# Kernel optimization log

Measured on AMD Instinct MI355X. Metric: run time of the kernel, lower is better.

## Reference

```python
import jax, jax.numpy as jnp
import numpy as np

EPS = 1e-5

def activation_quant(x):
    # per-token absmax int8 quant-dequant (BitNet b1.58)
    scale = 127.0 / jnp.clip(jnp.max(jnp.abs(x), axis=-1, keepdims=True), EPS)
    q = jnp.clip(jnp.round(x * scale), -128.0, 127.0) / scale
    return q

def weight_quant(w):
    # per-tensor ternary quant-dequant: scale by 1/mean|w|, round, clamp to {-1,0,1}
    scale = 1.0 / jnp.clip(jnp.mean(jnp.abs(w)), EPS)
    q = jnp.clip(jnp.round(w * scale), -1.0, 1.0) / scale
    return q

def bitlinear(x, w):
    # x: [b, s, in], w: [out, in] (nn.Linear layout)
    return jnp.einsum('bsi,oi->bso', activation_quant(x), weight_quant(w))

def setup_inputs() -> dict:
    key = jax.random.key(0)
    k1, k2, k3, k4 = jax.random.split(key, 4)
    B, S, H, I = 2, 2048, 4096, 11008
    x = jax.random.normal(k1, (B, S, H), dtype=jnp.float32)
    w_gate = jax.random.normal(k2, (I, H), dtype=jnp.float32) * (1.0 / np.sqrt(H))
    w_up = jax.random.normal(k3, (I, H), dtype=jnp.float32) * (1.0 / np.sqrt(H))
    w_down = jax.random.normal(k4, (H, I), dtype=jnp.float32) * (1.0 / np.sqrt(I))
    return {"x": x, "w_gate": w_gate, "w_up": w_up, "w_down": w_down}

def reference(x, w_gate, w_up, w_down):
    g = bitlinear(x, w_gate)           # [B, S, I]
    u = bitlinear(x, w_up)             # [B, S, I]
    h = jnp.square(jax.nn.relu(g)) * u  # ReLU^2 gating
    return bitlinear(h, w_down)        # [B, S, H]
```

## Files before the change

### kernel.cpp

```cpp
#include <hip/hip_runtime.h>
#include <stdint.h>

#define TOKENS 4096
#define HDIM   4096
#define IDIM   11008
#define WELEMS 45088768L

using i32x4 = __attribute__((ext_vector_type(4))) int;
using s8x16 = __attribute__((ext_vector_type(16))) signed char;

__device__ __forceinline__ void async_load16(const void* g, void* l) {
  __builtin_amdgcn_global_load_lds(
      (const __attribute__((address_space(1))) void*)g,
      (__attribute__((address_space(3))) void*)l, 16, 0, 0);
}

__global__ __launch_bounds__(256) void wsum_kernel(
    const float* __restrict__ w0, const float* __restrict__ w1,
    const float* __restrict__ w2, double* __restrict__ dsum) {
  const float* w = (blockIdx.y == 0) ? w0 : (blockIdx.y == 1) ? w1 : w2;
  const long n4 = WELEMS / 4;
  long i = (long)blockIdx.x * blockDim.x + threadIdx.x;
  const long stride = (long)gridDim.x * blockDim.x;
  double s = 0.0;
  for (; i < n4; i += stride) {
    float4 v = ((const float4*)w)[i];
    s += (double)fabsf(v.x); s += (double)fabsf(v.y);
    s += (double)fabsf(v.z); s += (double)fabsf(v.w);
  }
  __shared__ double red[256];
  red[threadIdx.x] = s;
  __syncthreads();
  for (int off = 128; off; off >>= 1) {
    if (threadIdx.x < (unsigned)off) red[threadIdx.x] += red[threadIdx.x + off];
    __syncthreads();
  }
  if (threadIdx.x == 0) atomicAdd(&dsum[blockIdx.y], red[0]);
}

__global__ void wscale_kernel(const double* __restrict__ dsum, double* __restrict__ wsc) {
  int i = threadIdx.x;
  if (i < 3) {
    double mean = dsum[i] / (double)WELEMS;
    wsc[i] = 1.0 / fmax(mean, 1e-5);
  }
}

__global__ __launch_bounds__(256) void wquant_kernel(
    const float* __restrict__ w0, const float* __restrict__ w1, const float* __restrict__ w2,
    int8_t* __restrict__ q0, int8_t* __restrict__ q1, int8_t* __restrict__ q2,
    const double* __restrict__ wsc) {
  const int wi = blockIdx.y;
  const float* w = (wi == 0) ? w0 : (wi == 1) ? w1 : w2;
  int8_t* q = (wi == 0) ? q0 : (wi == 1) ? q1 : q2;
  const double sc = wsc[wi];
  long c = (long)blockIdx.x * blockDim.x + threadIdx.x;
  if (c * 16 >= WELEMS) return;
  const float4* src = (const float4*)(w + c * 16);
  s8x16 outv;
  #pragma unroll
  for (int j = 0; j < 4; ++j) {
    float4 v = src[j];
    double t0 = rint((double)v.x * sc); t0 = fmin(fmax(t0, -1.0), 1.0);
    double t1 = rint((double)v.y * sc); t1 = fmin(fmax(t1, -1.0), 1.0);
    double t2 = rint((double)v.z * sc); t2 = fmin(fmax(t2, -1.0), 1.0);
    double t3 = rint((double)v.w * sc); t3 = fmin(fmax(t3, -1.0), 1.0);
    outv[j*4+0] = (signed char)(int)t0; outv[j*4+1] = (signed char)(int)t1;
    outv[j*4+2] = (signed char)(int)t2; outv[j*4+3] = (signed char)(int)t3;
  }
  *(s8x16*)(q + c * 16) = outv;
}

__global__ __launch_bounds__(256) void xquant_kernel(
    const float* __restrict__ x, int8_t* __restrict__ xq, double* __restrict__ sx) {
  const int row = blockIdx.x;
  const float* xr = x + (long)row * HDIM;
  const float4* xr4 = (const float4*)xr;
  float m = 0.f;
  for (int i = threadIdx.x; i < HDIM / 4; i += 256) {
    float4 v = xr4[i];
    m = fmaxf(m, fmaxf(fmaxf(fabsf(v.x), fabsf(v.y)), fmaxf(fabsf(v.z), fabsf(v.w))));
  }
  __shared__ float red[256];
  red[threadIdx.x] = m;
  __syncthreads();
  for (int off = 128; off; off >>= 1) {
    if (threadIdx.x < (unsigned)off) red[threadIdx.x] = fmaxf(red[threadIdx.x], red[threadIdx.x + off]);
    __syncthreads();
  }
  __shared__ double s_sc;
  if (threadIdx.x == 0) {
    double sc = 127.0 / fmax((double)red[0], 1e-5);
    sx[row] = sc;
    s_sc = sc;
  }
  __syncthreads();
  const double sc = s_sc;
  s8x16 outv;
  #pragma unroll
  for (int j = 0; j < 4; ++j) {
    float4 v = xr4[threadIdx.x * 4 + j];
    double t0 = rint((double)v.x * sc); t0 = fmin(fmax(t0, -128.0), 127.0);
    double t1 = rint((double)v.y * sc); t1 = fmin(fmax(t1, -128.0), 127.0);
    double t2 = rint((double)v.z * sc); t2 = fmin(fmax(t2, -128.0), 127.0);
    double t3 = rint((double)v.w * sc); t3 = fmin(fmax(t3, -128.0), 127.0);
    outv[j*4+0] = (signed char)(int)t0; outv[j*4+1] = (signed char)(int)t1;
    outv[j*4+2] = (signed char)(int)t2; outv[j*4+3] = (signed char)(int)t3;
  }
  *(s8x16*)(xq + (long)row * HDIM + threadIdx.x * 16) = outv;
}

__global__ __launch_bounds__(256, 2) void gemm1_kernel(
    const int8_t* __restrict__ Aq, const int8_t* __restrict__ Bg, const int8_t* __restrict__ Bu,
    const double* __restrict__ sx, const double* __restrict__ wsc,
    float* __restrict__ H, unsigned int* __restrict__ hmax) {
  __shared__ __align__(16) int8_t As[128 * 64];
  __shared__ __align__(16) int8_t Bsg[128 * 64];
  __shared__ __align__(16) int8_t Bsu[128 * 64];
  __shared__ unsigned int smax[128];

  const int tid = threadIdx.x;
  const int l = tid & 63;
  const int wv = tid >> 6;
  const int wm = (wv >> 1) * 64;
  const int wn = (wv & 1) * 64;
  const int row0 = blockIdx.y * 128;
  const int col0 = blockIdx.x * 128;

  i32x4 accg[4][4], accu[4][4];
  #pragma unroll
  for (int i = 0; i < 4; i++)
    #pragma unroll
    for (int j = 0; j < 4; j++) { accg[i][j] = i32x4{0,0,0,0}; accu[i][j] = i32x4{0,0,0,0}; }

  const int off0 = tid * 16;
  const int rs = off0 >> 6;
  const int cs = off0 & 63;

  for (int k0 = 0; k0 < HDIM; k0 += 64) {
    #pragma unroll
    for (int s = 0; s < 2; ++s) {
      const int off = off0 + s * 4096;
      const int r = rs + s * 64;
      const long ga = (long)(row0 + r) * HDIM + k0 + cs;
      const long gb = (long)(col0 + r) * HDIM + k0 + cs;
      async_load16(Aq + ga, As + off);
      async_load16(Bg + gb, Bsg + off);
      async_load16(Bu + gb, Bsu + off);
    }
    __syncthreads();
    const int kq = (l >> 4) * 16;
    const int mr = l & 15;
    i32x4 af[4], bgf[4], buf_[4];
    #pragma unroll
    for (int t = 0; t < 4; t++) af[t] = *(const i32x4*)(As + (wm + t * 16 + mr) * 64 + kq);
    #pragma unroll
    for (int t = 0; t < 4; t++) {
      bgf[t] = *(const i32x4*)(Bsg + (wn + t * 16 + mr) * 64 + kq);
      buf_[t] = *(const i32x4*)(Bsu + (wn + t * 16 + mr) * 64 + kq);
    }
    #pragma unroll
    for (int mt = 0; mt < 4; mt++)
      #pragma unroll
      for (int nt = 0; nt < 4; nt++) {
        accg[mt][nt] = __builtin_amdgcn_mfma_i32_16x16x64_i8(af[mt], bgf[nt], accg[mt][nt], 0, 0, 0);
        accu[mt][nt] = __builtin_amdgcn_mfma_i32_16x16x64_i8(af[mt], buf_[nt], accu[mt][nt], 0, 0, 0);
      }
    __syncthreads();
  }

  if (tid < 128) smax[tid] = 0u;
  __syncthreads();
  const double swg = wsc[0], swu = wsc[1];
  #pragma unroll
  for (int mt = 0; mt < 4; mt++) {
    #pragma unroll
    for (int r = 0; r < 4; r++) {
      const int grow = wm + mt * 16 + (l >> 4) * 4 + r;
      const long growg = row0 + grow;
      const double sxr = sx[growg];
      const double dg = 1.0 / (sxr * swg);
      const double du = 1.0 / (sxr * swu);
      float am = 0.f;
      #pragma unroll
      for (int nt = 0; nt < 4; nt++) {
        const float g = (float)((double)accg[mt][nt][r] * dg);
        const float u = (float)((double)accu[mt][nt][r] * du);
        const float gr = g > 0.f ? g * g : 0.f;
        const float h = gr * u;
        H[growg * IDIM + col0 + wn + nt * 16 + (l & 15)] = h;
        am = fmaxf(am, fabsf(h));
      }
      atomicMax(&smax[grow], __float_as_uint(am));
    }
  }
  __syncthreads();
  if (tid < 128) atomicMax(&hmax[row0 + tid], smax[tid]);
}

__global__ __launch_bounds__(256) void hquant_kernel(
    const float* __restrict__ H, int8_t* __restrict__ hq, const unsigned int* __restrict__ hmax) {
  const long c = (long)blockIdx.x * blockDim.x + threadIdx.x;
  const long nchunks = (long)TOKENS * IDIM / 16;
  if (c >= nchunks) return;
  const int row = (int)(c / (IDIM / 16));
  const double sc = 127.0 / fmax((double)__uint_as_float(hmax[row]), 1e-5);
  const float4* src = (const float4*)(H + c * 16);
  s8x16 outv;
  #pragma unroll
  for (int j = 0; j < 4; ++j) {
    float4 v = src[j];
    double t0 = rint((double)v.x * sc); t0 = fmin(fmax(t0, -128.0), 127.0);
    double t1 = rint((double)v.y * sc); t1 = fmin(fmax(t1, -128.0), 127.0);
    double t2 = rint((double)v.z * sc); t2 = fmin(fmax(t2, -128.0), 127.0);
    double t3 = rint((double)v.w * sc); t3 = fmin(fmax(t3, -128.0), 127.0);
    outv[j*4+0] = (signed char)(int)t0; outv[j*4+1] = (signed char)(int)t1;
    outv[j*4+2] = (signed char)(int)t2; outv[j*4+3] = (signed char)(int)t3;
  }
  *(s8x16*)(hq + c * 16) = outv;
}

__global__ __launch_bounds__(256, 2) void gemm2_kernel(
    const int8_t* __restrict__ Aq, const int8_t* __restrict__ Bq,
    const unsigned int* __restrict__ hmax, const double* __restrict__ wsc,
    float* __restrict__ out) {
  __shared__ __align__(16) int8_t As[128 * 64];
  __shared__ __align__(16) int8_t Bs[128 * 64];

  const int tid = threadIdx.x;
  const int l = tid & 63;
  const int wv = tid >> 6;
  const int wm = (wv >> 1) * 64;
  const int wn = (wv & 1) * 64;
  const int row0 = blockIdx.y * 128;
  const int col0 = blockIdx.x * 128;

  i32x4 acc[4][4];
  #pragma unroll
  for (int i = 0; i < 4; i++)
    #pragma unroll
    for (int j = 0; j < 4; j++) acc[i][j] = i32x4{0,0,0,0};

  const int off0 = tid * 16;
  const int rs = off0 >> 6;
  const int cs = off0 & 63;

  for (int k0 = 0; k0 < IDIM; k0 += 64) {
    #pragma unroll
    for (int s = 0; s < 2; ++s) {
      const int off = off0 + s * 4096;
      const int r = rs + s * 64;
      const long ga = (long)(row0 + r) * IDIM + k0 + cs;
      const long gb = (long)(col0 + r) * IDIM + k0 + cs;
      async_load16(Aq + ga, As + off);
      async_load16(Bq + gb, Bs + off);
    }
    __syncthreads();
    const int kq = (l >> 4) * 16;
    const int mr = l & 15;
    i32x4 af[4], bf[4];
    #pragma unroll
    for (int t = 0; t < 4; t++) af[t] = *(const i32x4*)(As + (wm + t * 16 + mr) * 64 + kq);
    #pragma unroll
    for (int t = 0; t < 4; t++) bf[t] = *(const i32x4*)(Bs + (wn + t * 16 + mr) * 64 + kq);
    #pragma unroll
    for (int mt = 0; mt < 4; mt++)
      #pragma unroll
      for (int nt = 0; nt < 4; nt++)
        acc[mt][nt] = __builtin_amdgcn_mfma_i32_16x16x64_i8(af[mt], bf[nt], acc[mt][nt], 0, 0, 0);
    __syncthreads();
  }

  const double swd = wsc[2];
  #pragma unroll
  for (int mt = 0; mt < 4; mt++) {
    #pragma unroll
    for (int r = 0; r < 4; r++) {
      const int grow = wm + mt * 16 + (l >> 4) * 4 + r;
      const long growg = row0 + grow;
      const double shr = 127.0 / fmax((double)__uint_as_float(hmax[growg]), 1e-5);
      const double inv = 1.0 / (shr * swd);
      #pragma unroll
      for (int nt = 0; nt < 4; nt++)
        out[growg * HDIM + col0 + wn + nt * 16 + (l & 15)] = (float)((double)acc[mt][nt][r] * inv);
    }
  }
}

extern "C" void kernel_launch(void* const* d_in, const int* in_sizes, int n_in,
                              void* d_out, int out_size, void* d_ws, size_t ws_size,
                              hipStream_t stream) {
  const float* x  = (const float*)d_in[0];
  const float* wg = (const float*)d_in[1];
  const float* wu = (const float*)d_in[2];
  const float* wd = (const float*)d_in[3];
  float* out = (float*)d_out;

  char* ws = (char*)d_ws;
  double*   dsum  = (double*)ws;
  double*   wsc   = (double*)(ws + 32);
  double*   sx    = (double*)(ws + 64);
  unsigned* hmaxb = (unsigned*)(ws + 64 + TOKENS * 8);
  int8_t*   xq    = (int8_t*)(ws + 131072);
  int8_t*   wqg   = xq + (long)TOKENS * HDIM;
  int8_t*   wqu   = wqg + WELEMS;
  int8_t*   wqd   = wqu + WELEMS;
  int8_t*   hq    = wqd + WELEMS;
  float*    H     = (float*)(hq + WELEMS);
  const size_t needed = 131072 + (size_t)TOKENS * HDIM + 4 * (size_t)WELEMS
                      + (size_t)TOKENS * IDIM * sizeof(float);
  if (ws_size < needed) {
    hipMemsetAsync(d_out, 0, (size_t)out_size * sizeof(float), stream);
    return;
  }

  hipMemsetAsync(ws, 0, 65536, stream);

  { dim3 g(1024, 3); wsum_kernel<<<g, 256, 0, stream>>>(wg, wu, wd, dsum); }
  wscale_kernel<<<1, 64, 0, stream>>>(dsum, wsc);
  { dim3 g((unsigned)(WELEMS / (256 * 16)), 3);
    wquant_kernel<<<g, 256, 0, stream>>>(wg, wu, wd, wqg, wqu, wqd, wsc); }
  xquant_kernel<<<TOKENS, 256, 0, stream>>>(x, xq, sx);
  { dim3 g(IDIM / 128, TOKENS / 128);
    gemm1_kernel<<<g, 256, 0, stream>>>(xq, wqg, wqu, sx, wsc, H, hmaxb); }
  hquant_kernel<<<(unsigned)((long)TOKENS * IDIM / 16 / 256), 256, 0, stream>>>(H, hq, hmaxb);
  { dim3 g(HDIM / 128, TOKENS / 128);
    gemm2_kernel<<<g, 256, 0, stream>>>(hq, wqd, hmaxb, wsc, out); }
}
```

Measured before the change: 1.386 ms.

## Use 32x32x32 int8 MFMA with XOR-swizzled LDS and swapped grid order

```diff
diff --git a/kernel.cpp b/kernel.cpp
--- a/kernel.cpp
+++ b/kernel.cpp
@@ -6,8 +6,9 @@
 #define IDIM   11008
 #define WELEMS 45088768L
 
-using i32x4 = __attribute__((ext_vector_type(4))) int;
-using s8x16 = __attribute__((ext_vector_type(16))) signed char;
+using i32x4  = __attribute__((ext_vector_type(4))) int;
+using i32x16 = __attribute__((ext_vector_type(16))) int;
+using s8x16  = __attribute__((ext_vector_type(16))) signed char;
 
 __device__ __forceinline__ void async_load16(const void* g, void* l) {
   __builtin_amdgcn_global_load_lds(
@@ -120,52 +121,65 @@
   __shared__ unsigned int smax[128];
 
   const int tid = threadIdx.x;
-  const int l = tid & 63;
+  const int l  = tid & 63;
   const int wv = tid >> 6;
   const int wm = (wv >> 1) * 64;
   const int wn = (wv & 1) * 64;
-  const int row0 = blockIdx.y * 128;
-  const int col0 = blockIdx.x * 128;
-
-  i32x4 accg[4][4], accu[4][4];
-  #pragma unroll
-  for (int i = 0; i < 4; i++)
-    #pragma unroll
-    for (int j = 0; j < 4; j++) { accg[i][j] = i32x4{0,0,0,0}; accu[i][j] = i32x4{0,0,0,0}; }
+  const int lr = l & 31;
+  const int lh = l >> 5;
+  const int row0 = blockIdx.x * 128;
+  const int col0 = blockIdx.y * 128;
+
+  i32x16 accg[2][2], accu[2][2];
+  #pragma unroll
+  for (int i = 0; i < 2; i++)
+    #pragma unroll
+    for (int j = 0; j < 2; j++) {
+      #pragma unroll
+      for (int e = 0; e < 16; e++) { accg[i][j][e] = 0; accu[i][j][e] = 0; }
+    }
 
   const int off0 = tid * 16;
-  const int rs = off0 >> 6;
-  const int cs = off0 & 63;
+  const int rs = tid >> 2;
+  const int ch = tid & 3;
+  const int csw = (ch ^ ((rs >> 1) & 3)) * 16;
 
   for (int k0 = 0; k0 < HDIM; k0 += 64) {
     #pragma unroll
     for (int s = 0; s < 2; ++s) {
       const int off = off0 + s * 4096;
       const int r = rs + s * 64;
-      const long ga = (long)(row0 + r) * HDIM + k0 + cs;
-      const long gb = (long)(col0 + r) * HDIM + k0 + cs;
+      const long ga = (long)(row0 + r) * HDIM + k0 + csw;
+      const long gb = (long)(col0 + r) * HDIM + k0 + csw;
       async_load16(Aq + ga, As + off);
       async_load16(Bg + gb, Bsg + off);
       async_load16(Bu + gb, Bsu + off);
     }
     __syncthreads();
-    const int kq = (l >> 4) * 16;
-    const int mr = l & 15;
-    i32x4 af[4], bgf[4], buf_[4];
-    #pragma unroll
-    for (int t = 0; t < 4; t++) af[t] = *(const i32x4*)(As + (wm + t * 16 + mr) * 64 + kq);
-    #pragma unroll
-    for (int t = 0; t < 4; t++) {
-      bgf[t] = *(const i32x4*)(Bsg + (wn + t * 16 + mr) * 64 + kq);
-      buf_[t] = *(const i32x4*)(Bsu + (wn + t * 16 + mr) * 64 + kq);
-    }
-    #pragma unroll
-    for (int mt = 0; mt < 4; mt++)
-      #pragma unroll
-      for (int nt = 0; nt < 4; nt++) {
-        accg[mt][nt] = __builtin_amdgcn_mfma_i32_16x16x64_i8(af[mt], bgf[nt], accg[mt][nt], 0, 0, 0);
-        accu[mt][nt] = __builtin_amdgcn_mfma_i32_16x16x64_i8(af[mt], buf_[nt], accu[mt][nt], 0, 0, 0);
-      }
+    #pragma unroll
+    for (int ks = 0; ks < 2; ++ks) {
+      const int c0 = ks * 2 + lh;
+      i32x4 af[2], bgf[2], buf_[2];
+      #pragma unroll
+      for (int t = 0; t < 2; t++) {
+        const int ra = wm + t * 32 + lr;
+        af[t] = *(const i32x4*)(As + ra * 64 + ((c0 ^ ((ra >> 1) & 3)) * 16));
+      }
+      #pragma unroll
+      for (int t = 0; t < 2; t++) {
+        const int rb = wn + t * 32 + lr;
+        const int cb = (c0 ^ ((rb >> 1) & 3)) * 16;
+        bgf[t]  = *(const i32x4*)(Bsg + rb * 64 + cb);
+        buf_[t] = *(const i32x4*)(Bsu + rb * 64 + cb);
+      }
+      #pragma unroll
+      for (int mt = 0; mt < 2; mt++)
+        #pragma unroll
+        for (int nt = 0; nt < 2; nt++) {
+          accg[mt][nt] = __builtin_amdgcn_mfma_i32_32x32x32_i8(af[mt], bgf[nt],  accg[mt][nt], 0, 0, 0);
+          accu[mt][nt] = __builtin_amdgcn_mfma_i32_32x32x32_i8(af[mt], buf_[nt], accu[mt][nt], 0, 0, 0);
+        }
+    }
     __syncthreads();
   }
 
@@ -173,25 +187,25 @@
   __syncthreads();
   const double swg = wsc[0], swu = wsc[1];
   #pragma unroll
-  for (int mt = 0; mt < 4; mt++) {
-    #pragma unroll
-    for (int r = 0; r < 4; r++) {
-      const int grow = wm + mt * 16 + (l >> 4) * 4 + r;
-      const long growg = row0 + grow;
+  for (int mt = 0; mt < 2; mt++) {
+    #pragma unroll
+    for (int reg = 0; reg < 16; reg++) {
+      const int rl = wm + mt * 32 + (reg & 3) + 8 * (reg >> 2) + 4 * lh;
+      const long growg = row0 + rl;
       const double sxr = sx[growg];
       const double dg = 1.0 / (sxr * swg);
       const double du = 1.0 / (sxr * swu);
       float am = 0.f;
       #pragma unroll
-      for (int nt = 0; nt < 4; nt++) {
-        const float g = (float)((double)accg[mt][nt][r] * dg);
-        const float u = (float)((double)accu[mt][nt][r] * du);
+      for (int nt = 0; nt < 2; nt++) {
+        const float g = (float)((double)accg[mt][nt][reg] * dg);
+        const float u = (float)((double)accu[mt][nt][reg] * du);
         const float gr = g > 0.f ? g * g : 0.f;
         const float h = gr * u;
-        H[growg * IDIM + col0 + wn + nt * 16 + (l & 15)] = h;
+        H[growg * IDIM + col0 + wn + nt * 32 + lr] = h;
         am = fmaxf(am, fabsf(h));
       }
-      atomicMax(&smax[grow], __float_as_uint(am));
+      atomicMax(&smax[rl], __float_as_uint(am));
     }
   }
   __syncthreads();
@@ -228,61 +242,75 @@
   __shared__ __align__(16) int8_t Bs[128 * 64];
 
   const int tid = threadIdx.x;
-  const int l = tid & 63;
+  const int l  = tid & 63;
   const int wv = tid >> 6;
   const int wm = (wv >> 1) * 64;
   const int wn = (wv & 1) * 64;
-  const int row0 = blockIdx.y * 128;
-  const int col0 = blockIdx.x * 128;
-
-  i32x4 acc[4][4];
-  #pragma unroll
-  for (int i = 0; i < 4; i++)
-    #pragma unroll
-    for (int j = 0; j < 4; j++) acc[i][j] = i32x4{0,0,0,0};
+  const int lr = l & 31;
+  const int lh = l >> 5;
+  const int row0 = blockIdx.x * 128;
+  const int col0 = blockIdx.y * 128;
+
+  i32x16 acc[2][2];
+  #pragma unroll
+  for (int i = 0; i < 2; i++)
+    #pragma unroll
+    for (int j = 0; j < 2; j++) {
+      #pragma unroll
+      for (int e = 0; e < 16; e++) acc[i][j][e] = 0;
+    }
 
   const int off0 = tid * 16;
-  const int rs = off0 >> 6;
-  const int cs = off0 & 63;
+  const int rs = tid >> 2;
+  const int ch = tid & 3;
+  const int csw = (ch ^ ((rs >> 1) & 3)) * 16;
 
   for (int k0 = 0; k0 < IDIM; k0 += 64) {
     #pragma unroll
     for (int s = 0; s < 2; ++s) {
       const int off = off0 + s * 4096;
       const int r = rs + s * 64;
-      const long ga = (long)(row0 + r) * IDIM + k0 + cs;
-      const long gb = (long)(col0 + r) * IDIM + k0 + cs;
+      const long ga = (long)(row0 + r) * IDIM + k0 + csw;
+      const long gb = (long)(col0 + r) * IDIM + k0 + csw;
       async_load16(Aq + ga, As + off);
       async_load16(Bq + gb, Bs + off);
     }
     __syncthreads();
-    const int kq = (l >> 4) * 16;
-    const int mr = l & 15;
-    i32x4 af[4], bf[4];
-    #pragma unroll
-    for (int t = 0; t < 4; t++) af[t] = *(const i32x4*)(As + (wm + t * 16 + mr) * 64 + kq);
-    #pragma unroll
-    for (int t = 0; t < 4; t++) bf[t] = *(const i32x4*)(Bs + (wn + t * 16 + mr) * 64 + kq);
-    #pragma unroll
-    for (int mt = 0; mt < 4; mt++)
-      #pragma unroll
-      for (int nt = 0; nt < 4; nt++)
-        acc[mt][nt] = __builtin_amdgcn_mfma_i32_16x16x64_i8(af[mt], bf[nt], acc[mt][nt], 0, 0, 0);
+    #pragma unroll
+    for (int ks = 0; ks < 2; ++ks) {
+      const int c0 = ks * 2 + lh;
+      i32x4 af[2], bf[2];
+      #pragma unroll
+      for (int t = 0; t < 2; t++) {
+        const int ra = wm + t * 32 + lr;
+        af[t] = *(const i32x4*)(As + ra * 64 + ((c0 ^ ((ra >> 1) & 3)) * 16));
+      }
+      #pragma unroll
+      for (int t = 0; t < 2; t++) {
+        const int rb = wn + t * 32 + lr;
+        bf[t] = *(const i32x4*)(Bs + rb * 64 + ((c0 ^ ((rb >> 1) & 3)) * 16));
+      }
+      #pragma unroll
+      for (int mt = 0; mt < 2; mt++)
+        #pragma unroll
+        for (int nt = 0; nt < 2; nt++)
+          acc[mt][nt] = __builtin_amdgcn_mfma_i32_32x32x32_i8(af[mt], bf[nt], acc[mt][nt], 0, 0, 0);
+    }
     __syncthreads();
   }
 
   const double swd = wsc[2];
   #pragma unroll
-  for (int mt = 0; mt < 4; mt++) {
-    #pragma unroll
-    for (int r = 0; r < 4; r++) {
-      const int grow = wm + mt * 16 + (l >> 4) * 4 + r;
-      const long growg = row0 + grow;
+  for (int mt = 0; mt < 2; mt++) {
+    #pragma unroll
+    for (int reg = 0; reg < 16; reg++) {
+      const int rl = wm + mt * 32 + (reg & 3) + 8 * (reg >> 2) + 4 * lh;
+      const long growg = row0 + rl;
       const double shr = 127.0 / fmax((double)__uint_as_float(hmax[growg]), 1e-5);
       const double inv = 1.0 / (shr * swd);
       #pragma unroll
-      for (int nt = 0; nt < 4; nt++)
-        out[growg * HDIM + col0 + wn + nt * 16 + (l & 15)] = (float)((double)acc[mt][nt][r] * inv);
+      for (int nt = 0; nt < 2; nt++)
+        out[growg * HDIM + col0 + wn + nt * 32 + lr] = (float)((double)acc[mt][nt][reg] * inv);
     }
   }
 }
@@ -321,9 +349,9 @@
   { dim3 g((unsigned)(WELEMS / (256 * 16)), 3);
     wquant_kernel<<<g, 256, 0, stream>>>(wg, wu, wd, wqg, wqu, wqd, wsc); }
   xquant_kernel<<<TOKENS, 256, 0, stream>>>(x, xq, sx);
-  { dim3 g(IDIM / 128, TOKENS / 128);
+  { dim3 g(TOKENS / 128, IDIM / 128);
     gemm1_kernel<<<g, 256, 0, stream>>>(xq, wqg, wqu, sx, wsc, H, hmaxb); }
   hquant_kernel<<<(unsigned)((long)TOKENS * IDIM / 16 / 256), 256, 0, stream>>>(H, hq, hmaxb);
-  { dim3 g(HDIM / 128, TOKENS / 128);
+  { dim3 g(TOKENS / 128, HDIM / 128);
     gemm2_kernel<<<g, 256, 0, stream>>>(hq, wqd, hmaxb, wsc, out); }
 }
```

Measured after the change: 1.413 ms. Within noise of the previous version (+1.9%).
